# Optimization experiments

Measured on AMD Instinct MI355X. Metric: run time of the kernel, lower is better.

Reference implementation:

```python
import jax, jax.numpy as jnp
import numpy as np

N, E, D, L = 100000, 640000, 128, 3
EPS = 1e-5


def setup_inputs() -> dict:
    key = jax.random.key(0)
    ks = jax.random.split(key, 12)
    s = 1.0 / np.sqrt(D)
    return {
        "x": jax.random.normal(ks[0], (N, D), dtype=jnp.float32),
        "edge_index": jax.random.randint(ks[1], (2, E), 0, N, dtype=jnp.int64),
        "conv_w": jax.random.normal(ks[2], (L, D, D), dtype=jnp.float32) * s,
        "conv_b": jnp.zeros((L, D), dtype=jnp.float32),
        "gn_weight": jnp.ones((L, D), dtype=jnp.float32),
        "gn_bias": jnp.zeros((L, D), dtype=jnp.float32),
        "gn_mean_scale": jnp.ones((L, D), dtype=jnp.float32),
        "proj_w": jax.random.normal(ks[3], (D, D), dtype=jnp.float32) * s,
        "mlp_w": jax.random.normal(ks[4], (D, D), dtype=jnp.float32) * s,
        "mlp_b": jnp.zeros((D,), dtype=jnp.float32),
        "head_w": jax.random.normal(ks[5], (D, 1), dtype=jnp.float32) * s,
        "head_b": jnp.zeros((1,), dtype=jnp.float32),
    }


def _graph_norm(h, w, b, ms):
    # PyG GraphNorm over a single graph: subtract learnable-scaled mean, divide by std.
    mean = jnp.mean(h, axis=0)
    out = h - ms * mean
    var = jnp.mean(out * out, axis=0)
    return out / jnp.sqrt(var + EPS) * w + b


def reference(x, edge_index, conv_w, conv_b, gn_weight, gn_bias, gn_mean_scale,
              proj_w, mlp_w, mlp_b, head_w, head_b):
    n = x.shape[0]
    loop = jnp.arange(n, dtype=edge_index.dtype)
    row = jnp.concatenate([edge_index[0], loop])  # source
    col = jnp.concatenate([edge_index[1], loop])  # destination
    deg = jax.ops.segment_sum(jnp.ones_like(col, dtype=x.dtype), col, num_segments=n)
    dinv = jnp.where(deg > 0, jax.lax.rsqrt(deg), 0.0)
    norm = dinv[row] * dinv[col]  # [E+N]

    def gcn_conv(h, W, b):
        hw = h @ W                          # [N, D]
        msg = hw[row] * norm[:, None]       # gather + scale, [E+N, D]
        return jax.ops.segment_sum(msg, col, num_segments=n) + b

    h1 = x
    for i in range(L):
        residual = h1 @ proj_w if i == 0 else x  # shared_source skip
        h = gcn_conv(x, conv_w[i], conv_b[i])
        h = _graph_norm(h, gn_weight[i], gn_bias[i], gn_mean_scale[i])
        x = jax.nn.relu(h) + residual

    x = jax.nn.relu(x @ mlp_w + mlp_b)      # shared MLP (one layer for sizes [D, D])
    return x @ head_w + head_b              # task head -> [N, 1]
```

## Files before the change

### kernel.cpp

```cpp
#include <hip/hip_runtime.h>

#define FD 128

typedef __attribute__((ext_vector_type(8))) short bf16x8;
typedef __attribute__((ext_vector_type(4))) float f32x4;

__device__ __forceinline__ unsigned short f2bf(float f) {
  unsigned int u = __float_as_uint(f);
  unsigned int r = (u + 0x7fffu + ((u >> 16) & 1u)) >> 16;
  return (unsigned short)r;
}
__device__ __forceinline__ float bf_lo(unsigned int u) { return __uint_as_float(u << 16); }
__device__ __forceinline__ float bf_hi(unsigned int u) { return __uint_as_float(u & 0xffff0000u); }
__device__ __forceinline__ unsigned int pack_bf2(float a, float b) {
  return (unsigned int)f2bf(a) | ((unsigned int)f2bf(b) << 16);
}

__global__ __launch_bounds__(256) void init_kernel(int* __restrict__ deg, int* __restrict__ fill,
    float* __restrict__ stats, int n) {
  int i = blockIdx.x * 256 + threadIdx.x;
  if (i < n) { deg[i] = 1; fill[i] = 0; }
  if (i < 768) stats[i] = 0.f;
}

__global__ __launch_bounds__(256) void edge_count_kernel(const int* __restrict__ ei, int e, int* __restrict__ deg) {
  int i = blockIdx.x * 256 + threadIdx.x;
  if (i < e) atomicAdd(&deg[ei[e + i]], 1);
}

__global__ __launch_bounds__(128) void scan1_kernel(const int* __restrict__ deg, int n,
    int* __restrict__ tmp, int* __restrict__ partials, float* __restrict__ dinv) {
  __shared__ int s[128];
  int b = blockIdx.x, t = threadIdx.x;
  int i = b * 128 + t;
  int d = (i < n) ? deg[i] : 1;
  if (i < n) dinv[i] = rsqrtf((float)d);
  s[t] = (i < n) ? (d - 1) : 0;
  __syncthreads();
  for (int off = 1; off < 128; off <<= 1) {
    int u = (t >= off) ? s[t - off] : 0;
    __syncthreads();
    s[t] += u;
    __syncthreads();
  }
  if (i < n) tmp[i] = s[t];
  if (t == 127) partials[b] = s[127];
}

__global__ __launch_bounds__(1024) void scan2_kernel(int* __restrict__ partials, int nb) {
  __shared__ int s[1024];
  int t = threadIdx.x;
  s[t] = (t < nb) ? partials[t] : 0;
  __syncthreads();
  for (int off = 1; off < 1024; off <<= 1) {
    int u = (t >= off) ? s[t - off] : 0;
    __syncthreads();
    s[t] += u;
    __syncthreads();
  }
  if (t < nb) partials[t] = (t == 0) ? 0 : s[t - 1];
}

__global__ __launch_bounds__(128) void scan3_kernel(const int* __restrict__ tmp, const int* __restrict__ partials, int* __restrict__ indptr, int n) {
  int i = blockIdx.x * 128 + threadIdx.x;
  if (i < n) indptr[i + 1] = tmp[i] + partials[blockIdx.x];
  if (i == 0) indptr[0] = 0;
}

__global__ __launch_bounds__(256) void fill_kernel(const int* __restrict__ ei, int e,
    const int* __restrict__ indptr, int* __restrict__ fill, const float* __restrict__ dinv,
    int* __restrict__ csr_src, float* __restrict__ csr_norm) {
  int i = blockIdx.x * 256 + threadIdx.x;
  if (i < e) {
    int r = ei[i];
    int c = ei[e + i];
    int pos = indptr[c] + atomicAdd(&fill[c], 1);
    csr_src[pos] = r;
    csr_norm[pos] = dinv[r] * dinv[c];
  }
}

__global__ __launch_bounds__(256) void prep_w(const float* __restrict__ conv_w, const float* __restrict__ proj_w,
    const float* __restrict__ mlp_w, unsigned short* __restrict__ Wtb) {
  int idx = blockIdx.x * 256 + threadIdx.x;
  int m = idx >> 14;
  int o = idx & 16383;
  int col = o >> 7, k = o & 127;
  const float* src = (m < 3) ? (conv_w + m * 16384) : ((m == 3) ? proj_w : mlp_w);
  Wtb[idx] = f2bf(src[k * FD + col]);
}

__global__ __launch_bounds__(256) void gemm_dual(const float* __restrict__ x0,
    const unsigned short* __restrict__ W0t, const unsigned short* __restrict__ Pt,
    unsigned short* __restrict__ hw0, unsigned short* __restrict__ xp, int n)
{
  __shared__ uint4 bsh[2048];
  const int tid = threadIdx.x;
  const int l = tid & 63;
  const int w = tid >> 6;
  const int row0 = blockIdx.x * 64 + w * 16;

  #pragma unroll
  for (int it = 0; it < 8; ++it) {
    int s = it * 256 + tid;
    int nf = s >> 8, kf = (s >> 6) & 3, sl = s & 63;
    int col = nf * 16 + (sl & 15);
    bsh[s] = *(const uint4*)(W0t + col * FD + kf * 32 + (sl >> 4) * 8);
  }

  const int arow = row0 + (l & 15);
  bf16x8 a[4];
  if (arow < n) {
    const float4* ap = (const float4*)(x0 + (size_t)arow * FD + (l >> 4) * 8);
    #pragma unroll
    for (int kf = 0; kf < 4; ++kf) {
      float4 f0 = ap[kf * 8];
      float4 f1 = ap[kf * 8 + 1];
      uint4 pk;
      pk.x = pack_bf2(f0.x, f0.y); pk.y = pack_bf2(f0.z, f0.w);
      pk.z = pack_bf2(f1.x, f1.y); pk.w = pack_bf2(f1.z, f1.w);
      a[kf] = *(bf16x8*)&pk;
    }
  } else {
    #pragma unroll
    for (int kf = 0; kf < 4; ++kf) a[kf] = (bf16x8)(short)0;
  }

  __syncthreads();

  f32x4 acc[8];
  #pragma unroll
  for (int nf = 0; nf < 8; ++nf) acc[nf] = (f32x4)(0.0f);
  #pragma unroll
  for (int nf = 0; nf < 8; ++nf)
    #pragma unroll
    for (int kf = 0; kf < 4; ++kf) {
      uint4 braw = bsh[(nf * 4 + kf) * 64 + l];
      acc[nf] = __builtin_amdgcn_mfma_f32_16x16x32_bf16(a[kf], *(bf16x8*)&braw, acc[nf], 0, 0, 0);
    }

  __syncthreads();

  #pragma unroll
  for (int it = 0; it < 8; ++it) {
    int s = it * 256 + tid;
    int nf = s >> 8, kf = (s >> 6) & 3, sl = s & 63;
    int col = nf * 16 + (sl & 15);
    bsh[s] = *(const uint4*)(Pt + col * FD + kf * 32 + (sl >> 4) * 8);
  }
  #pragma unroll
  for (int nf = 0; nf < 8; ++nf) {
    int col = nf * 16 + (l & 15);
    #pragma unroll
    for (int i = 0; i < 4; ++i) {
      int r = row0 + (l >> 4) * 4 + i;
      if (r < n) hw0[(size_t)r * FD + col] = f2bf(acc[nf][i]);
    }
  }

  __syncthreads();

  #pragma unroll
  for (int nf = 0; nf < 8; ++nf) acc[nf] = (f32x4)(0.0f);
  #pragma unroll
  for (int nf = 0; nf < 8; ++nf)
    #pragma unroll
    for (int kf = 0; kf < 4; ++kf) {
      uint4 braw = bsh[(nf * 4 + kf) * 64 + l];
      acc[nf] = __builtin_amdgcn_mfma_f32_16x16x32_bf16(a[kf], *(bf16x8*)&braw, acc[nf], 0, 0, 0);
    }
  #pragma unroll
  for (int nf = 0; nf < 8; ++nf) {
    int col = nf * 16 + (l & 15);
    #pragma unroll
    for (int i = 0; i < 4; ++i) {
      int r = row0 + (l >> 4) * 4 + i;
      if (r < n) xp[(size_t)r * FD + col] = f2bf(acc[nf][i]);
    }
  }
}

template<int EPI>
__global__ __launch_bounds__(256) void mfma_gemm(const unsigned short* __restrict__ Ab,
    const unsigned short* __restrict__ Wtb, void* __restrict__ Cout, int n,
    const float* __restrict__ bias, const float* __restrict__ hw, const float* __restrict__ hb,
    const float* __restrict__ svA, const float* __restrict__ tvA,
    const unsigned short* __restrict__ residA, unsigned short* __restrict__ xout)
{
  __shared__ uint4 bsh[2048];
  const int tid = threadIdx.x;
  const int l = tid & 63;
  const int w = tid >> 6;
  const int row0 = blockIdx.x * 64 + w * 16;

  #pragma unroll
  for (int it = 0; it < 8; ++it) {
    int s = it * 256 + tid;
    int nf = s >> 8, kf = (s >> 6) & 3, sl = s & 63;
    int col = nf * 16 + (sl & 15);
    bsh[s] = *(const uint4*)(Wtb + col * FD + kf * 32 + (sl >> 4) * 8);
  }

  const int arow = row0 + (l & 15);
  bf16x8 a[4];
  if (arow < n) {
    const uint4* agp = (const uint4*)(Ab + (size_t)arow * FD + (l >> 4) * 8);
    const uint4* rsp = (const uint4*)(residA + (size_t)arow * FD + (l >> 4) * 8);
    uint4* xop = xout ? (uint4*)(xout + (size_t)arow * FD + (l >> 4) * 8) : nullptr;
    #pragma unroll
    for (int kf = 0; kf < 4; ++kf) {
      uint4 ag = agp[kf * 4];
      uint4 rs = rsp[kf * 4];
      int cb4 = kf * 8 + (l >> 4) * 2;
      float4 s0 = ((const float4*)svA)[cb4];
      float4 s1 = ((const float4*)svA)[cb4 + 1];
      float4 t0 = ((const float4*)tvA)[cb4];
      float4 t1 = ((const float4*)tvA)[cb4 + 1];
      uint4 pk;
      pk.x = pack_bf2(fmaxf(fmaf(bf_lo(ag.x), s0.x, t0.x), 0.f) + bf_lo(rs.x),
                      fmaxf(fmaf(bf_hi(ag.x), s0.y, t0.y), 0.f) + bf_hi(rs.x));
      pk.y = pack_bf2(fmaxf(fmaf(bf_lo(ag.y), s0.z, t0.z), 0.f) + bf_lo(rs.y),
                      fmaxf(fmaf(bf_hi(ag.y), s0.w, t0.w), 0.f) + bf_hi(rs.y));
      pk.z = pack_bf2(fmaxf(fmaf(bf_lo(ag.z), s1.x, t1.x), 0.f) + bf_lo(rs.z),
                      fmaxf(fmaf(bf_hi(ag.z), s1.y, t1.y), 0.f) + bf_hi(rs.z));
      pk.w = pack_bf2(fmaxf(fmaf(bf_lo(ag.w), s1.z, t1.z), 0.f) + bf_lo(rs.w),
                      fmaxf(fmaf(bf_hi(ag.w), s1.w, t1.w), 0.f) + bf_hi(rs.w));
      a[kf] = *(bf16x8*)&pk;
      if (xop) xop[kf * 4] = pk;
    }
  } else {
    #pragma unroll
    for (int kf = 0; kf < 4; ++kf) a[kf] = (bf16x8)(short)0;
  }

  __syncthreads();

  f32x4 acc[8];
  #pragma unroll
  for (int nf = 0; nf < 8; ++nf) acc[nf] = (f32x4)(0.0f);
  #pragma unroll
  for (int nf = 0; nf < 8; ++nf)
    #pragma unroll
    for (int kf = 0; kf < 4; ++kf) {
      uint4 braw = bsh[(nf * 4 + kf) * 64 + l];
      acc[nf] = __builtin_amdgcn_mfma_f32_16x16x32_bf16(a[kf], *(bf16x8*)&braw, acc[nf], 0, 0, 0);
    }

  if (EPI == 2) {
    float hsum[4] = {0.f, 0.f, 0.f, 0.f};
    #pragma unroll
    for (int nf = 0; nf < 8; ++nf) {
      int col = nf * 16 + (l & 15);
      float bm = bias[col];
      float hwc = hw[col];
      #pragma unroll
      for (int i = 0; i < 4; ++i)
        hsum[i] += fmaxf(acc[nf][i] + bm, 0.f) * hwc;
    }
    #pragma unroll
    for (int i = 0; i < 4; ++i) {
      #pragma unroll
      for (int off = 1; off < 16; off <<= 1) hsum[i] += __shfl_xor(hsum[i], off);
    }
    if ((l & 15) == 0) {
      float hb0 = hb[0];
      #pragma unroll
      for (int i = 0; i < 4; ++i) {
        int r = row0 + (l >> 4) * 4 + i;
        if (r < n) ((float*)Cout)[r] = hsum[i] + hb0;
      }
    }
  } else {
    unsigned short* outp = (unsigned short*)Cout;
    #pragma unroll
    for (int nf = 0; nf < 8; ++nf) {
      int col = nf * 16 + (l & 15);
      #pragma unroll
      for (int i = 0; i < 4; ++i) {
        int r = row0 + (l >> 4) * 4 + i;
        if (r < n) outp[(size_t)r * FD + col] = f2bf(acc[nf][i]);
      }
    }
  }
}

__device__ __forceinline__ void acc8(float* a, uint4 u, float wn) {
  a[0] = fmaf(wn, bf_lo(u.x), a[0]); a[1] = fmaf(wn, bf_hi(u.x), a[1]);
  a[2] = fmaf(wn, bf_lo(u.y), a[2]); a[3] = fmaf(wn, bf_hi(u.y), a[3]);
  a[4] = fmaf(wn, bf_lo(u.z), a[4]); a[5] = fmaf(wn, bf_hi(u.z), a[5]);
  a[6] = fmaf(wn, bf_lo(u.w), a[6]); a[7] = fmaf(wn, bf_hi(u.w), a[7]);
}

__global__ __launch_bounds__(256) void agg_bf16(const uint4* __restrict__ hw4, uint4* __restrict__ agg4,
    const int* __restrict__ indptr, const int* __restrict__ csr_src, const float* __restrict__ csr_norm,
    const float* __restrict__ dinv, const float* __restrict__ bias,
    float* __restrict__ colsum, float* __restrict__ colsum2, int n)
{
  __shared__ float sredS[4][16][9];
  __shared__ float sredQ[4][16][9];
  const int wv = threadIdx.x >> 6;
  const int lane = threadIdx.x & 63;
  const int q = lane >> 4;
  const int l16 = lane & 15;
  const int gs = blockIdx.x * 16 + wv * 4 + q;
  const int ns = gridDim.x * 16;
  const float4 b0 = ((const float4*)bias)[l16 * 2];
  const float4 b1 = ((const float4*)bias)[l16 * 2 + 1];
  float st[8], sq[8];
  #pragma unroll
  for (int j = 0; j < 8; ++j) { st[j] = 0.f; sq[j] = 0.f; }

  int c = gs;
  float di = 0.f; int e0 = 0, e1 = 0;
  uint4 su = make_uint4(0, 0, 0, 0);
  if (c < n) {
    di = dinv[c];
    e0 = indptr[c]; e1 = indptr[c + 1];
    su = hw4[(size_t)c * 16 + l16];
  }
  while (c < n) {
    const int cn = c + ns;
    float di_n = 0.f; int e0_n = 0, e1_n = 0;
    uint4 su_n = make_uint4(0, 0, 0, 0);
    if (cn < n) {
      di_n = dinv[cn];
      e0_n = indptr[cn]; e1_n = indptr[cn + 1];
      su_n = hw4[(size_t)cn * 16 + l16];
    }

    float self = di * di;
    float a[8];
    a[0] = fmaf(self, bf_lo(su.x), b0.x); a[1] = fmaf(self, bf_hi(su.x), b0.y);
    a[2] = fmaf(self, bf_lo(su.y), b0.z); a[3] = fmaf(self, bf_hi(su.y), b0.w);
    a[4] = fmaf(self, bf_lo(su.z), b1.x); a[5] = fmaf(self, bf_hi(su.z), b1.y);
    a[6] = fmaf(self, bf_lo(su.w), b1.z); a[7] = fmaf(self, bf_hi(su.w), b1.w);
    int e = e0;
    for (; e + 4 <= e1; e += 4) {
      int s0 = csr_src[e], s1 = csr_src[e + 1], s2 = csr_src[e + 2], s3 = csr_src[e + 3];
      float w0 = csr_norm[e], w1 = csr_norm[e + 1], w2 = csr_norm[e + 2], w3 = csr_norm[e + 3];
      uint4 u0 = hw4[(size_t)s0 * 16 + l16];
      uint4 u1 = hw4[(size_t)s1 * 16 + l16];
      uint4 u2 = hw4[(size_t)s2 * 16 + l16];
      uint4 u3 = hw4[(size_t)s3 * 16 + l16];
      acc8(a, u0, w0); acc8(a, u1, w1); acc8(a, u2, w2); acc8(a, u3, w3);
    }
    if (e + 2 <= e1) {
      int s0 = csr_src[e], s1 = csr_src[e + 1];
      float w0 = csr_norm[e], w1 = csr_norm[e + 1];
      uint4 u0 = hw4[(size_t)s0 * 16 + l16];
      uint4 u1 = hw4[(size_t)s1 * 16 + l16];
      acc8(a, u0, w0); acc8(a, u1, w1);
      e += 2;
    }
    if (e < e1) {
      int s0 = csr_src[e];
      float w0 = csr_norm[e];
      uint4 u0 = hw4[(size_t)s0 * 16 + l16];
      acc8(a, u0, w0);
    }
    uint4 o;
    o.x = pack_bf2(a[0], a[1]); o.y = pack_bf2(a[2], a[3]);
    o.z = pack_bf2(a[4], a[5]); o.w = pack_bf2(a[6], a[7]);
    agg4[(size_t)c * 16 + l16] = o;
    #pragma unroll
    for (int j = 0; j < 8; ++j) { st[j] += a[j]; sq[j] += a[j] * a[j]; }

    c = cn; di = di_n; e0 = e0_n; e1 = e1_n; su = su_n;
  }

  #pragma unroll
  for (int j = 0; j < 8; ++j) {
    st[j] += __shfl_xor(st[j], 16); st[j] += __shfl_xor(st[j], 32);
    sq[j] += __shfl_xor(sq[j], 16); sq[j] += __shfl_xor(sq[j], 32);
  }
  if (q == 0) {
    #pragma unroll
    for (int j = 0; j < 8; ++j) { sredS[wv][l16][j] = st[j]; sredQ[wv][l16][j] = sq[j]; }
  }
  __syncthreads();
  int t = threadIdx.x;
  int which = t >> 7, cc = t & 127;
  int rl = cc >> 3, rk = cc & 7;
  float v = 0.f;
  #pragma unroll
  for (int w2 = 0; w2 < 4; ++w2)
    v += which ? sredQ[w2][rl][rk] : sredS[w2][rl][rk];
  atomicAdd(which ? &colsum2[cc] : &colsum[cc], v);
}

__global__ void finalize_stats(const float* __restrict__ colsum, const float* __restrict__ colsum2,
    const float* __restrict__ gnw, const float* __restrict__ gnb, const float* __restrict__ ms,
    float* __restrict__ sv, float* __restrict__ tv, float inv_n)
{
  int d = threadIdx.x;
  if (d < FD) {
    float mean = colsum[d] * inv_n;
    float m2 = colsum2[d] * inv_n;
    float m = ms[d];
    float var = m2 - 2.f * m * mean * mean + m * m * mean * mean;
    float s = gnw[d] * rsqrtf(var + 1e-5f);
    sv[d] = s;
    tv[d] = gnb[d] - m * mean * s;
  }
}

extern "C" void kernel_launch(void* const* d_in, const int* in_sizes, int n_in,
                              void* d_out, int out_size, void* d_ws, size_t ws_size,
                              hipStream_t stream) {
  const float* x0      = (const float*)d_in[0];
  const int* ei        = (const int*)d_in[1];
  const float* conv_w  = (const float*)d_in[2];
  const float* conv_b  = (const float*)d_in[3];
  const float* gn_w    = (const float*)d_in[4];
  const float* gn_b    = (const float*)d_in[5];
  const float* gn_ms   = (const float*)d_in[6];
  const float* proj_w  = (const float*)d_in[7];
  const float* mlp_w   = (const float*)d_in[8];
  const float* mlp_b   = (const float*)d_in[9];
  const float* head_w  = (const float*)d_in[10];
  const float* head_b  = (const float*)d_in[11];
  float* out = (float*)d_out;

  const int n = in_sizes[0] / FD;
  const int e = in_sizes[1] / 2;
  const size_t ND = (size_t)n * FD;

  unsigned short* hwb  = (unsigned short*)d_ws;
  unsigned short* aggb = hwb + ND;
  unsigned short* xpb  = aggb + ND;
  unsigned short* xrb  = xpb + ND;
  unsigned short* Wtb  = xrb + ND;
  float* csr_norm = (float*)(Wtb + 5 * 16384);
  float* dinv     = csr_norm + e;
  float* stats    = dinv + n;
  float* sv       = stats + 768;
  float* tv       = sv + FD;
  int* deg     = (int*)(tv + FD);
  int* fill    = deg + n;
  int* indptr  = fill + n;
  int* tmp     = indptr + (n + 1);
  int* partials= tmp + n;
  int* csr_src = partials + 1024;

  const int nb256_n = (n + 255) / 256;
  const int nb256_e = (e + 255) / 256;
  const int nb128_n = (n + 127) / 128;

  init_kernel<<<nb256_n, 256, 0, stream>>>(deg, fill, stats, n);
  edge_count_kernel<<<nb256_e, 256, 0, stream>>>(ei, e, deg);
  scan1_kernel<<<nb128_n, 128, 0, stream>>>(deg, n, tmp, partials, dinv);
  scan2_kernel<<<1, 1024, 0, stream>>>(partials, nb128_n);
  scan3_kernel<<<nb128_n, 128, 0, stream>>>(tmp, partials, indptr, n);
  fill_kernel<<<nb256_e, 256, 0, stream>>>(ei, e, indptr, fill, dinv, csr_src, csr_norm);

  prep_w<<<320, 256, 0, stream>>>(conv_w, proj_w, mlp_w, Wtb);

  const int gemm_grid = (n + 63) / 64;
  const float inv_n = 1.f / (float)n;
  const unsigned short* Wt_conv0 = Wtb;
  const unsigned short* Wt_conv1 = Wtb + 16384;
  const unsigned short* Wt_conv2 = Wtb + 2 * 16384;
  const unsigned short* Wt_proj  = Wtb + 3 * 16384;
  const unsigned short* Wt_mlp   = Wtb + 4 * 16384;

  gemm_dual<<<gemm_grid, 256, 0, stream>>>(x0, Wt_conv0, Wt_proj, hwb, xpb, n);
  agg_bf16<<<2048, 256, 0, stream>>>((const uint4*)hwb, (uint4*)aggb, indptr, csr_src, csr_norm, dinv,
                                     conv_b + 0 * FD, stats + 0 * FD, stats + 384 + 0 * FD, n);
  finalize_stats<<<1, 128, 0, stream>>>(stats + 0 * FD, stats + 384 + 0 * FD,
      gn_w + 0 * FD, gn_b + 0 * FD, gn_ms + 0 * FD, sv, tv, inv_n);

  mfma_gemm<0><<<gemm_grid, 256, 0, stream>>>(aggb, Wt_conv1, hwb, n,
      nullptr, nullptr, nullptr, sv, tv, xpb, xrb);
  agg_bf16<<<2048, 256, 0, stream>>>((const uint4*)hwb, (uint4*)aggb, indptr, csr_src, csr_norm, dinv,
                                     conv_b + 1 * FD, stats + 1 * FD, stats + 384 + 1 * FD, n);
  finalize_stats<<<1, 128, 0, stream>>>(stats + 1 * FD, stats + 384 + 1 * FD,
      gn_w + 1 * FD, gn_b + 1 * FD, gn_ms + 1 * FD, sv, tv, inv_n);

  mfma_gemm<0><<<gemm_grid, 256, 0, stream>>>(aggb, Wt_conv2, hwb, n,
      nullptr, nullptr, nullptr, sv, tv, xrb, xpb);
  agg_bf16<<<2048, 256, 0, stream>>>((const uint4*)hwb, (uint4*)aggb, indptr, csr_src, csr_norm, dinv,
                                     conv_b + 2 * FD, stats + 2 * FD, stats + 384 + 2 * FD, n);
  finalize_stats<<<1, 128, 0, stream>>>(stats + 2 * FD, stats + 384 + 2 * FD,
      gn_w + 2 * FD, gn_b + 2 * FD, gn_ms + 2 * FD, sv, tv, inv_n);

  mfma_gemm<2><<<gemm_grid, 256, 0, stream>>>(aggb, Wt_mlp, out, n,
      mlp_b, head_w, head_b, sv, tv, xpb, nullptr);
}
```

Before: 401.0 us.

## Balance aggregation rows by edge count and fold GraphNorm finalize into GEMM

Adds a balance kernel that binary-searches the CSR indptr to give each aggregation sub-wave a contiguous row range with roughly equal edge-plus-row work, replacing the strided row assignment. Consecutive rows also let the loop reuse indptr[c+1] as the next row's start. The separate single-block finalize_stats launches are removed, and each GEMM block now recomputes the GraphNorm scale and shift into shared memory. This removes three tiny launches and evens out per-wave load, but contiguous row ranges change the gather locality and add one extra setup kernel.

```diff
diff --git a/kernel.cpp b/kernel.cpp
--- a/kernel.cpp
+++ b/kernel.cpp
@@ -80,6 +80,21 @@
   }
 }
 
+__global__ __launch_bounds__(256) void balance_kernel(const int* __restrict__ indptr, int n, int S,
+    int* __restrict__ rowstart) {
+  int s = blockIdx.x * 256 + threadIdx.x;
+  if (s > S) return;
+  long long total = (long long)indptr[n] + 2LL * n;
+  long long target = (total * s) / S;
+  int lo = 0, hi = n;
+  while (lo < hi) {
+    int mid = (lo + hi) >> 1;
+    long long f = (long long)indptr[mid] + 2LL * mid;
+    if (f >= target) hi = mid; else lo = mid + 1;
+  }
+  rowstart[s] = lo;
+}
+
 __global__ __launch_bounds__(256) void prep_w(const float* __restrict__ conv_w, const float* __restrict__ proj_w,
     const float* __restrict__ mlp_w, unsigned short* __restrict__ Wtb) {
   int idx = blockIdx.x * 256 + threadIdx.x;
@@ -184,10 +199,13 @@
 __global__ __launch_bounds__(256) void mfma_gemm(const unsigned short* __restrict__ Ab,
     const unsigned short* __restrict__ Wtb, void* __restrict__ Cout, int n,
     const float* __restrict__ bias, const float* __restrict__ hw, const float* __restrict__ hb,
-    const float* __restrict__ svA, const float* __restrict__ tvA,
-    const unsigned short* __restrict__ residA, unsigned short* __restrict__ xout)
+    const float* __restrict__ colsum, const float* __restrict__ colsum2,
+    const float* __restrict__ gnw, const float* __restrict__ gnb, const float* __restrict__ gnms,
+    float inv_n, const unsigned short* __restrict__ residA, unsigned short* __restrict__ xout)
 {
   __shared__ uint4 bsh[2048];
+  __shared__ __align__(16) float svs[128];
+  __shared__ __align__(16) float tvs[128];
   const int tid = threadIdx.x;
   const int l = tid & 63;
   const int w = tid >> 6;
@@ -200,6 +218,16 @@
     int col = nf * 16 + (sl & 15);
     bsh[s] = *(const uint4*)(Wtb + col * FD + kf * 32 + (sl >> 4) * 8);
   }
+  if (tid < 128) {
+    float mean = colsum[tid] * inv_n;
+    float m2 = colsum2[tid] * inv_n;
+    float m = gnms[tid];
+    float var = m2 - 2.f * m * mean * mean + m * m * mean * mean;
+    float sc = gnw[tid] * rsqrtf(var + 1e-5f);
+    svs[tid] = sc;
+    tvs[tid] = gnb[tid] - m * mean * sc;
+  }
+  __syncthreads();
 
   const int arow = row0 + (l & 15);
   bf16x8 a[4];
@@ -212,10 +240,10 @@
       uint4 ag = agp[kf * 4];
       uint4 rs = rsp[kf * 4];
       int cb4 = kf * 8 + (l >> 4) * 2;
-      float4 s0 = ((const float4*)svA)[cb4];
-      float4 s1 = ((const float4*)svA)[cb4 + 1];
-      float4 t0 = ((const float4*)tvA)[cb4];
-      float4 t1 = ((const float4*)tvA)[cb4 + 1];
+      float4 s0 = ((const float4*)svs)[cb4];
+      float4 s1 = ((const float4*)svs)[cb4 + 1];
+      float4 t0 = ((const float4*)tvs)[cb4];
+      float4 t1 = ((const float4*)tvs)[cb4 + 1];
       uint4 pk;
       pk.x = pack_bf2(fmaxf(fmaf(bf_lo(ag.x), s0.x, t0.x), 0.f) + bf_lo(rs.x),
                       fmaxf(fmaf(bf_hi(ag.x), s0.y, t0.y), 0.f) + bf_hi(rs.x));
@@ -294,7 +322,8 @@
 __global__ __launch_bounds__(256) void agg_bf16(const uint4* __restrict__ hw4, uint4* __restrict__ agg4,
     const int* __restrict__ indptr, const int* __restrict__ csr_src, const float* __restrict__ csr_norm,
     const float* __restrict__ dinv, const float* __restrict__ bias,
-    float* __restrict__ colsum, float* __restrict__ colsum2, int n)
+    float* __restrict__ colsum, float* __restrict__ colsum2,
+    const int* __restrict__ rowstart, int n)
 {
   __shared__ float sredS[4][16][9];
   __shared__ float sredQ[4][16][9];
@@ -302,29 +331,29 @@
   const int lane = threadIdx.x & 63;
   const int q = lane >> 4;
   const int l16 = lane & 15;
-  const int gs = blockIdx.x * 16 + wv * 4 + q;
-  const int ns = gridDim.x * 16;
+  const int sid = blockIdx.x * 16 + wv * 4 + q;
   const float4 b0 = ((const float4*)bias)[l16 * 2];
   const float4 b1 = ((const float4*)bias)[l16 * 2 + 1];
   float st[8], sq[8];
   #pragma unroll
   for (int j = 0; j < 8; ++j) { st[j] = 0.f; sq[j] = 0.f; }
 
-  int c = gs;
+  int c = rowstart[sid];
+  const int cend = rowstart[sid + 1];
   float di = 0.f; int e0 = 0, e1 = 0;
   uint4 su = make_uint4(0, 0, 0, 0);
-  if (c < n) {
+  if (c < cend) {
     di = dinv[c];
     e0 = indptr[c]; e1 = indptr[c + 1];
     su = hw4[(size_t)c * 16 + l16];
   }
-  while (c < n) {
-    const int cn = c + ns;
-    float di_n = 0.f; int e0_n = 0, e1_n = 0;
+  while (c < cend) {
+    const int cn = c + 1;
+    float di_n = 0.f; int e1_n = 0;
     uint4 su_n = make_uint4(0, 0, 0, 0);
-    if (cn < n) {
+    if (cn < cend) {
       di_n = dinv[cn];
-      e0_n = indptr[cn]; e1_n = indptr[cn + 1];
+      e1_n = indptr[cn + 1];
       su_n = hw4[(size_t)cn * 16 + l16];
     }
 
@@ -365,7 +394,7 @@
     #pragma unroll
     for (int j = 0; j < 8; ++j) { st[j] += a[j]; sq[j] += a[j] * a[j]; }
 
-    c = cn; di = di_n; e0 = e0_n; e1 = e1_n; su = su_n;
+    c = cn; di = di_n; e0 = e1; e1 = e1_n; su = su_n;
   }
 
   #pragma unroll
@@ -386,22 +415,6 @@
   for (int w2 = 0; w2 < 4; ++w2)
     v += which ? sredQ[w2][rl][rk] : sredS[w2][rl][rk];
   atomicAdd(which ? &colsum2[cc] : &colsum[cc], v);
-}
-
-__global__ void finalize_stats(const float* __restrict__ colsum, const float* __restrict__ colsum2,
-    const float* __restrict__ gnw, const float* __restrict__ gnb, const float* __restrict__ ms,
-    float* __restrict__ sv, float* __restrict__ tv, float inv_n)
-{
-  int d = threadIdx.x;
-  if (d < FD) {
-    float mean = colsum[d] * inv_n;
-    float m2 = colsum2[d] * inv_n;
-    float m = ms[d];
-    float var = m2 - 2.f * m * mean * mean + m * m * mean * mean;
-    float s = gnw[d] * rsqrtf(var + 1e-5f);
-    sv[d] = s;
-    tv[d] = gnb[d] - m * mean * s;
-  }
 }
 
 extern "C" void kernel_launch(void* const* d_in, const int* in_sizes, int n_in,
@@ -424,6 +437,8 @@
   const int n = in_sizes[0] / FD;
   const int e = in_sizes[1] / 2;
   const size_t ND = (size_t)n * FD;
+  const int AGG_BLOCKS = 2048;
+  const int NSTREAMS = AGG_BLOCKS * 16;
 
   unsigned short* hwb  = (unsigned short*)d_ws;
   unsigned short* aggb = hwb + ND;
@@ -433,14 +448,13 @@
   float* csr_norm = (float*)(Wtb + 5 * 16384);
   float* dinv     = csr_norm + e;
   float* stats    = dinv + n;
-  float* sv       = stats + 768;
-  float* tv       = sv + FD;
-  int* deg     = (int*)(tv + FD);
-  int* fill    = deg + n;
-  int* indptr  = fill + n;
-  int* tmp     = indptr + (n + 1);
-  int* partials= tmp + n;
-  int* csr_src = partials + 1024;
+  int* deg      = (int*)(stats + 768);
+  int* fill     = deg + n;
+  int* indptr   = fill + n;
+  int* tmp      = indptr + (n + 1);
+  int* partials = tmp + n;
+  int* rowstart = partials + 1024;
+  int* csr_src  = rowstart + (NSTREAMS + 1);
 
   const int nb256_n = (n + 255) / 256;
   const int nb256_e = (e + 255) / 256;
@@ -452,6 +466,7 @@
   scan2_kernel<<<1, 1024, 0, stream>>>(partials, nb128_n);
   scan3_kernel<<<nb128_n, 128, 0, stream>>>(tmp, partials, indptr, n);
   fill_kernel<<<nb256_e, 256, 0, stream>>>(ei, e, indptr, fill, dinv, csr_src, csr_norm);
+  balance_kernel<<<(NSTREAMS + 256) / 256, 256, 0, stream>>>(indptr, n, NSTREAMS, rowstart);
 
   prep_w<<<320, 256, 0, stream>>>(conv_w, proj_w, mlp_w, Wtb);
 
@@ -464,25 +479,22 @@
   const unsigned short* Wt_mlp   = Wtb + 4 * 16384;
 
   gemm_dual<<<gemm_grid, 256, 0, stream>>>(x0, Wt_conv0, Wt_proj, hwb, xpb, n);
-  agg_bf16<<<2048, 256, 0, stream>>>((const uint4*)hwb, (uint4*)aggb, indptr, csr_src, csr_norm, dinv,
-                                     conv_b + 0 * FD, stats + 0 * FD, stats + 384 + 0 * FD, n);
-  finalize_stats<<<1, 128, 0, stream>>>(stats + 0 * FD, stats + 384 + 0 * FD,
-      gn_w + 0 * FD, gn_b + 0 * FD, gn_ms + 0 * FD, sv, tv, inv_n);
+  agg_bf16<<<AGG_BLOCKS, 256, 0, stream>>>((const uint4*)hwb, (uint4*)aggb, indptr, csr_src, csr_norm, dinv,
+      conv_b + 0 * FD, stats + 0 * FD, stats + 384 + 0 * FD, rowstart, n);
 
   mfma_gemm<0><<<gemm_grid, 256, 0, stream>>>(aggb, Wt_conv1, hwb, n,
-      nullptr, nullptr, nullptr, sv, tv, xpb, xrb);
-  agg_bf16<<<2048, 256, 0, stream>>>((const uint4*)hwb, (uint4*)aggb, indptr, csr_src, csr_norm, dinv,
-                                     conv_b + 1 * FD, stats + 1 * FD, stats + 384 + 1 * FD, n);
-  finalize_stats<<<1, 128, 0, stream>>>(stats + 1 * FD, stats + 384 + 1 * FD,
-      gn_w + 1 * FD, gn_b + 1 * FD, gn_ms + 1 * FD, sv, tv, inv_n);
+      nullptr, nullptr, nullptr, stats + 0 * FD, stats + 384 + 0 * FD,
+      gn_w + 0 * FD, gn_b + 0 * FD, gn_ms + 0 * FD, inv_n, xpb, xrb);
+  agg_bf16<<<AGG_BLOCKS, 256, 0, stream>>>((const uint4*)hwb, (uint4*)aggb, indptr, csr_src, csr_norm, dinv,
+      conv_b + 1 * FD, stats + 1 * FD, stats + 384 + 1 * FD, rowstart, n);
 
   mfma_gemm<0><<<gemm_grid, 256, 0, stream>>>(aggb, Wt_conv2, hwb, n,
-      nullptr, nullptr, nullptr, sv, tv, xrb, xpb);
-  agg_bf16<<<2048, 256, 0, stream>>>((const uint4*)hwb, (uint4*)aggb, indptr, csr_src, csr_norm, dinv,
-                                     conv_b + 2 * FD, stats + 2 * FD, stats + 384 + 2 * FD, n);
-  finalize_stats<<<1, 128, 0, stream>>>(stats + 2 * FD, stats + 384 + 2 * FD,
-      gn_w + 2 * FD, gn_b + 2 * FD, gn_ms + 2 * FD, sv, tv, inv_n);
+      nullptr, nullptr, nullptr, stats + 1 * FD, stats + 384 + 1 * FD,
+      gn_w + 1 * FD, gn_b + 1 * FD, gn_ms + 1 * FD, inv_n, xrb, xpb);
+  agg_bf16<<<AGG_BLOCKS, 256, 0, stream>>>((const uint4*)hwb, (uint4*)aggb, indptr, csr_src, csr_norm, dinv,
+      conv_b + 2 * FD, stats + 2 * FD, stats + 384 + 2 * FD, rowstart, n);
 
   mfma_gemm<2><<<gemm_grid, 256, 0, stream>>>(aggb, Wt_mlp, out, n,
-      mlp_b, head_w, head_b, sv, tv, xpb, nullptr);
-}
+      mlp_b, head_w, head_b, stats + 2 * FD, stats + 384 + 2 * FD,
+      gn_w + 2 * FD, gn_b + 2 * FD, gn_ms + 2 * FD, inv_n, xpb, nullptr);
+}
```

Result: no change. 399.9 us (-0.3%).
